# Kernel tuning notes

Hardware: AMD Instinct MI355X
Metric: run time of the kernel (lower is better)

The kernel has to match this reference:

```python
import jax, jax.numpy as jnp
import numpy as np

B, P, E, H = 2, 4096, 512, 8
D = E // H
EPS = 1e-5


def _layernorm2d(x, g, b):
    # LayerNorm over last two dims (patches, embed) jointly, per torch nn.LayerNorm([P, E])
    mu = jnp.mean(x, axis=(-2, -1), keepdims=True)
    var = jnp.mean(jnp.square(x - mu), axis=(-2, -1), keepdims=True)
    return (x - mu) * jax.lax.rsqrt(var + EPS) * g + b


def setup_inputs() -> dict:
    key = jax.random.key(0)
    ks = jax.random.split(key, 4)
    s_in = 1.0 / np.sqrt(E)
    s_hid = 1.0 / np.sqrt(3 * E)
    return {
        "x": jax.random.normal(ks[0], (B, P, E), dtype=jnp.float32),
        "g1": jnp.ones((P, E), jnp.float32),
        "b1": jnp.zeros((P, E), jnp.float32),
        "W1": jax.random.normal(ks[1], (3 * E, E), jnp.float32) * s_in,
        "g2": jnp.ones((P, E), jnp.float32),
        "b2": jnp.zeros((P, E), jnp.float32),
        "Wa": jax.random.normal(ks[2], (3 * E, E), jnp.float32) * s_in,
        "ba": jnp.zeros((3 * E,), jnp.float32),
        "Wb": jax.random.normal(ks[3], (E, 3 * E), jnp.float32) * s_hid,
        "bb": jnp.zeros((E,), jnp.float32),
    }


def reference(x, g1, b1, W1, g2, b2, Wa, ba, Wb, bb):
    # --- attention branch ---
    h = _layernorm2d(x, g1, b1)                      # [B,P,E]
    qkv = h @ W1.T                                   # [B,P,3E]
    qkv = qkv.reshape(B, P, 3, H, D).transpose(2, 0, 3, 1, 4)  # [3,B,H,P,D]
    q, k, v = qkv[0], qkv[1], qkv[2]
    scale = 1.0 / jnp.sqrt(jnp.float32(D))
    dp = jnp.einsum("bhqd,bhkd->bhqk", q, k) * scale  # [B,H,P,P]
    # NOTE: softmax over axis -2 (the query axis), as in the original code
    dp = jax.nn.softmax(dp, axis=-2)
    wv = jnp.einsum("bhqk,bhkd->bhqd", dp, v)        # [B,H,P,D]
    wv = wv.transpose(0, 2, 1, 3).reshape(B, P, E)   # [B,P,E]
    out1 = x + wv
    # --- MLP branch ---
    h2 = _layernorm2d(out1, g2, b2)
    h2 = jax.nn.gelu(h2 @ Wa.T + ba, approximate=False)
    h2 = jax.nn.gelu(h2 @ Wb.T + bb, approximate=False)
    return h2 + out1
```

## Files before the change

kernel.cpp:

```cpp
#include <hip/hip_runtime.h>
#include <math.h>

typedef __bf16 bf16x8 __attribute__((ext_vector_type(8)));
typedef __bf16 bf16x4 __attribute__((ext_vector_type(4)));
typedef short s16x4 __attribute__((ext_vector_type(4)));
typedef float f32x4 __attribute__((ext_vector_type(4)));
typedef unsigned int u32x2 __attribute__((ext_vector_type(2)));
typedef unsigned short u16;
typedef unsigned int u32;

__device__ __forceinline__ void gl_lds16(const void* g, void* l) {
  __builtin_amdgcn_global_load_lds(
      (const __attribute__((address_space(1))) void*)g,
      (__attribute__((address_space(3))) void*)l, 16, 0, 0);
}

__device__ __forceinline__ u16 f2bf(float x) {
  union { float f; u32 u; } v; v.f = x;
  u32 r = v.u + 0x7FFFu + ((v.u >> 16) & 1u);
  return (u16)(r >> 16);
}

__device__ __forceinline__ float bflo(u32 u) {
  union { float f; u32 v; } t; t.v = u << 16; return t.f;
}
__device__ __forceinline__ float bfhi(u32 u) {
  union { float f; u32 v; } t; t.v = u & 0xFFFF0000u; return t.f;
}

__device__ __forceinline__ u32 pack_bf2(float a, float b) {
  union { float f; u32 u; } ua, ub; ua.f = a; ub.f = b;
  return ((ua.u + 0x8000u) >> 16) | ((ub.u + 0x8000u) & 0xFFFF0000u);
}

__device__ __forceinline__ float expfast(float x) {
#if __has_builtin(__builtin_amdgcn_exp2f)
  return __builtin_amdgcn_exp2f(x);
#else
  return exp2f(x);
#endif
}

__device__ __forceinline__ f32x4 mfma16(bf16x4 a, bf16x4 b, f32x4 c) {
#if __has_builtin(__builtin_amdgcn_mfma_f32_16x16x16_bf16)
  return __builtin_amdgcn_mfma_f32_16x16x16_bf16(a, b, c, 0, 0, 0);
#else
  return __builtin_amdgcn_mfma_f32_16x16x16bf16_1k(
      __builtin_bit_cast(s16x4, a), __builtin_bit_cast(s16x4, b), c, 0, 0, 0);
#endif
}

__device__ __forceinline__ float gelu_f(float v) {
  return 0.5f * v * (1.0f + erff(v * 0.7071067811865475f));
}

__global__ void cast_lnred(const float* __restrict__ s0, const float* __restrict__ s1,
                           const float* __restrict__ s2, u16* __restrict__ d0,
                           u16* __restrict__ d1, u16* __restrict__ d2,
                           const float* __restrict__ x, float2* __restrict__ part) {
  int blk = blockIdx.x;
  if (blk < 2304) {
    const float* s; u16* d;
    if (blk < 768)       { s = s0; d = d0; }
    else if (blk < 1536) { s = s1; d = d1; blk -= 768; }
    else                 { s = s2; d = d2; blk -= 1536; }
    int i = blk * 256 + threadIdx.x;
    float4 v = ((const float4*)s)[i];
    uint2 o;
    o.x = (u32)f2bf(v.x) | ((u32)f2bf(v.y) << 16);
    o.y = (u32)f2bf(v.z) | ((u32)f2bf(v.w) << 16);
    ((uint2*)d)[i] = o;
    return;
  }
  blk -= 2304;
  int b = blk >> 7, ib = blk & 127;
  const float4* p = (const float4*)(x + (size_t)b * 2097152 + (size_t)ib * 16384);
  float s = 0.f, q = 0.f;
  #pragma unroll
  for (int i = 0; i < 16; i++) {
    float4 v = p[i * 256 + threadIdx.x];
    s += v.x + v.y + v.z + v.w;
    q += v.x * v.x + v.y * v.y + v.z * v.z + v.w * v.w;
  }
  #pragma unroll
  for (int off = 32; off; off >>= 1) { s += __shfl_down(s, off, 64); q += __shfl_down(q, off, 64); }
  __shared__ float ls[4], lq[4];
  int w = threadIdx.x >> 6;
  if ((threadIdx.x & 63) == 0) { ls[w] = s; lq[w] = q; }
  __syncthreads();
  if (threadIdx.x == 0)
    part[b * 128 + ib] =
        make_float2(ls[0] + ls[1] + ls[2] + ls[3], lq[0] + lq[1] + lq[2] + lq[3]);
}

__global__ void comb_lnred(const float* __restrict__ x, const u16* __restrict__ opart,
                           float* __restrict__ o1, float2* __restrict__ part) {
  int blk = blockIdx.x;
  size_t base = (size_t)blk * 4096;
  const uint2* oa = (const uint2*)opart;
  const uint2* ob = (const uint2*)(opart + 4194304);
  float s = 0.f, q = 0.f;
  #pragma unroll
  for (int i = 0; i < 16; i++) {
    size_t idx = base + i * 256 + threadIdx.x;
    float4 v = ((const float4*)x)[idx];
    uint2 a = oa[idx];
    uint2 c = ob[idx];
    v.x += bflo(a.x) + bflo(c.x);
    v.y += bfhi(a.x) + bfhi(c.x);
    v.z += bflo(a.y) + bflo(c.y);
    v.w += bfhi(a.y) + bfhi(c.y);
    ((float4*)o1)[idx] = v;
    s += v.x + v.y + v.z + v.w;
    q += v.x * v.x + v.y * v.y + v.z * v.z + v.w * v.w;
  }
  #pragma unroll
  for (int off = 32; off; off >>= 1) { s += __shfl_down(s, off, 64); q += __shfl_down(q, off, 64); }
  __shared__ float ls[4], lq[4];
  int w = threadIdx.x >> 6;
  if ((threadIdx.x & 63) == 0) { ls[w] = s; lq[w] = q; }
  __syncthreads();
  if (threadIdx.x == 0)
    part[blk] = make_float2(ls[0] + ls[1] + ls[2] + ls[3], lq[0] + lq[1] + lq[2] + lq[3]);
}

__global__ void ln_apply(const float* __restrict__ src, const float* __restrict__ g,
                         const float* __restrict__ bta, const float2* __restrict__ part,
                         u16* __restrict__ dst) {
  int i = blockIdx.x * 256 + threadIdx.x;
  int b = i >= 524288;
  int lane = threadIdx.x & 63;
  float2 a = part[b * 128 + lane], c2 = part[b * 128 + 64 + lane];
  float s = a.x + c2.x, q = a.y + c2.y;
  #pragma unroll
  for (int off = 32; off; off >>= 1) { s += __shfl_down(s, off, 64); q += __shfl_down(q, off, 64); }
  s = __shfl(s, 0, 64); q = __shfl(q, 0, 64);
  const float inv = 1.0f / 2097152.0f;
  float mu = s * inv;
  float rsig = rsqrtf(q * inv - mu * mu + 1e-5f);
  int r = i - b * 524288;
  float4 v = ((const float4*)src)[i];
  float4 gv = ((const float4*)g)[r];
  float4 bv = ((const float4*)bta)[r];
  float h0 = (v.x - mu) * rsig * gv.x + bv.x;
  float h1 = (v.y - mu) * rsig * gv.y + bv.y;
  float h2 = (v.z - mu) * rsig * gv.z + bv.z;
  float h3 = (v.w - mu) * rsig * gv.w + bv.w;
  uint2 o;
  o.x = (u32)f2bf(h0) | ((u32)f2bf(h1) << 16);
  o.y = (u32)f2bf(h2) | ((u32)f2bf(h3) << 16);
  ((uint2*)dst)[i] = o;
}

template <int MODE>
__global__ __launch_bounds__(256, 2)
void gemm_bt(const u16* __restrict__ A, const u16* __restrict__ Bm,
             const float* __restrict__ bias, const float* __restrict__ res,
             float* __restrict__ outf, u16* __restrict__ outb,
             int M, int N, int K) {
  __shared__ u16 As[128 * 32], Bs[128 * 32];
  const int tid = threadIdx.x;
  const int m0 = blockIdx.y * 128, n0 = blockIdx.x * 128;
  const int lane = tid & 63, w = tid >> 6;
  const int wm = (w >> 1) * 64, wn = (w & 1) * 64;
  const int c = lane & 15, quad = lane >> 4;
  const int arow = tid >> 2, acol = (tid & 3) * 8;

  const u16* gA = A + (size_t)(m0 + arow) * K + acol;
  const u16* gB = Bm + (size_t)(n0 + arow) * K + acol;
  u16* lA = As + tid * 8;
  u16* lB = Bs + tid * 8;

  f32x4 acc[4][4] = {};
  for (int kt = 0; kt < K; kt += 32) {
    gl_lds16(gA, lA);
    gl_lds16(gA + (size_t)64 * K, lA + 64 * 32);
    gl_lds16(gB, lB);
    gl_lds16(gB + (size_t)64 * K, lB + 64 * 32);
    gA += 32; gB += 32;
    __syncthreads();
    bf16x8 af[4], bf[4];
    #pragma unroll
    for (int i = 0; i < 4; i++) {
      af[i] = *(const bf16x8*)&As[(wm + i * 16 + c) * 32 + quad * 8];
      bf[i] = *(const bf16x8*)&Bs[(wn + i * 16 + c) * 32 + quad * 8];
    }
    #pragma unroll
    for (int i = 0; i < 4; i++)
      #pragma unroll
      for (int j = 0; j < 4; j++)
        acc[i][j] = __builtin_amdgcn_mfma_f32_16x16x32_bf16(af[i], bf[j], acc[i][j], 0, 0, 0);
    __syncthreads();
  }
  #pragma unroll
  for (int i = 0; i < 4; i++) {
    const int row0 = m0 + wm + i * 16 + quad * 4;
    #pragma unroll
    for (int j = 0; j < 4; j++) {
      const int col = n0 + wn + j * 16 + c;
      #pragma unroll
      for (int r = 0; r < 4; r++) {
        float v = acc[i][j][r];
        size_t oi = (size_t)(row0 + r) * N + col;
        if (MODE == 0 && col < 512) v *= 0.1803368801111204f;
        if (MODE == 1 || MODE == 2) v = gelu_f(v + bias[col]);
        if (MODE == 2) outf[oi] = v + res[oi];
        else           outb[oi] = f2bf(v);
      }
    }
  }
}

__global__ __launch_bounds__(256, 4)
void attn_pass1(const u16* __restrict__ qkv, float* __restrict__ rlpart) {
  __shared__ u16 Qs[2][2 * 128 * 32];
  const int tid = threadIdx.x;
  const int bh = blockIdx.y, b = bh >> 3, h = bh & 7;
  const int k0 = blockIdx.x * 128;
  const int lane = tid & 63, w = tid >> 6;
  const int wn = w * 32;
  const int c = lane & 15, quad = lane >> 4;
  const int arow = tid >> 2, acol = (tid & 3) * 8;

  bf16x8 bk[2][2];
  {
    const u16* Kg = qkv + ((size_t)(b * 4096 + k0 + wn + c)) * 1536 + 512 + h * 64 + quad * 8;
    #pragma unroll
    for (int j = 0; j < 2; j++)
      #pragma unroll
      for (int ks = 0; ks < 2; ks++)
        bk[j][ks] = *(const bf16x8*)(Kg + (size_t)j * 16 * 1536 + ks * 32);
  }
  const u16* Qg = qkv + ((size_t)(b * 4096 + blockIdx.z * 2048)) * 1536 + h * 64;

  #define STAGE_Q(t)                                                              \
    {                                                                             \
      u16* dst = Qs[(t) & 1];                                                     \
      const u16* src = Qg + (size_t)((t) * 128) * 1536;                           \
      _Pragma("unroll")                                                           \
      for (int ks = 0; ks < 2; ks++)                                              \
        _Pragma("unroll")                                                         \
        for (int rr = 0; rr < 128; rr += 64)                                      \
          gl_lds16(src + (size_t)(rr + arow) * 1536 + ks * 32 + acol,             \
                   dst + ks * 4096 + (rr + arow) * 32 + acol);                    \
    }

  STAGE_Q(0);
  float s0 = 0.f, s1 = 0.f;
  for (int t = 0; t < 16; t++) {
    __syncthreads();
    if (t + 1 < 16) STAGE_Q(t + 1);
    const u16* buf = Qs[t & 1];
    #pragma unroll
    for (int i = 0; i < 8; i++) {
      bf16x8 a0 = *(const bf16x8*)&buf[(i * 16 + c) * 32 + quad * 8];
      bf16x8 a1 = *(const bf16x8*)&buf[4096 + (i * 16 + c) * 32 + quad * 8];
      f32x4 acc0 = {}, acc1 = {};
      acc0 = __builtin_amdgcn_mfma_f32_16x16x32_bf16(a0, bk[0][0], acc0, 0, 0, 0);
      acc0 = __builtin_amdgcn_mfma_f32_16x16x32_bf16(a1, bk[0][1], acc0, 0, 0, 0);
      acc1 = __builtin_amdgcn_mfma_f32_16x16x32_bf16(a0, bk[1][0], acc1, 0, 0, 0);
      acc1 = __builtin_amdgcn_mfma_f32_16x16x32_bf16(a1, bk[1][1], acc1, 0, 0, 0);
      #pragma unroll
      for (int r = 0; r < 4; r++) {
        s0 += expfast(acc0[r]);
        s1 += expfast(acc1[r]);
      }
    }
  }
  #undef STAGE_Q
  s0 += __shfl_xor(s0, 16, 64); s0 += __shfl_xor(s0, 32, 64);
  s1 += __shfl_xor(s1, 16, 64); s1 += __shfl_xor(s1, 32, 64);
  if (quad == 0) {
    float* rp = rlpart + ((size_t)blockIdx.z * 16 + bh) * 4096 + k0 + wn;
    rp[c] = s0;
    rp[16 + c] = s1;
  }
}

__global__ void vtrans(const u16* __restrict__ qkv, const float* __restrict__ rlpart,
                       u16* __restrict__ vt) {
  __shared__ u16 t[64 * 66];
  __shared__ float rls[64];
  int bh = blockIdx.y, p0 = blockIdx.x * 64;
  int b = bh >> 3, h = bh & 7;
  const u16* src = qkv + ((size_t)(b * 4096 + p0)) * 1536 + 1024 + h * 64;
  int tid = threadIdx.x;
  if (tid < 64) {
    size_t idx = (size_t)bh * 4096 + p0 + tid;
    rls[tid] = 1.0f / (rlpart[idx] + rlpart[65536 + idx]);
  }
  __syncthreads();
  #pragma unroll
  for (int j = 0; j < 16; j++) {
    int idx = j * 256 + tid;
    int p = idx >> 6, d = idx & 63;
    union { float f; u32 u; } uv;
    uv.u = ((u32)src[(size_t)p * 1536 + d]) << 16;
    t[d * 66 + p] = f2bf(uv.f * rls[p]);
  }
  __syncthreads();
  u16* dst = vt + (size_t)bh * 262144 + (size_t)blockIdx.x * 4096;
  #pragma unroll
  for (int j = 0; j < 16; j++) {
    int idx = j * 256 + tid;
    int d = idx >> 6, p = idx & 63;
    dst[d * 64 + ((((p >> 3) & 7) ^ (d & 7)) << 3) + (p & 7)] = t[d * 66 + p];
  }
}

__global__ __launch_bounds__(256, 4)
void attn_pass2(const u16* __restrict__ qkv, const u16* __restrict__ vt,
                u16* __restrict__ opart) {
  __shared__ u16 Ks[2][2][2048];
  __shared__ u16 Vs[2][4096];
  const int tid = threadIdx.x;
  const int bh = blockIdx.y, b = bh >> 3, h = bh & 7;
  const int q0 = blockIdx.x * 128;
  const int kh = blockIdx.z;
  const int lane = tid & 63, w = tid >> 6;
  const int wq = w * 32;
  const int c = lane & 15, quad = lane >> 4;

  bf16x8 bq[2][2];
  {
    const u16* Qg = qkv + ((size_t)(b * 4096 + q0 + wq + c)) * 1536 + h * 64 + quad * 8;
    #pragma unroll
    for (int j = 0; j < 2; j++)
      #pragma unroll
      for (int ks = 0; ks < 2; ks++)
        bq[j][ks] = *(const bf16x8*)(Qg + (size_t)j * 16 * 1536 + ks * 32);
  }
  const u16* Kg = qkv + ((size_t)(b * 4096 + kh * 2048)) * 1536 + 512 + h * 64;
  const u16* Vg = vt + (size_t)bh * 262144 + (size_t)kh * 131072;

  #define STAGE_KV(t)                                                             \
    {                                                                             \
      const int buf_ = (t) & 1;                                                   \
      const int krow_ = (t) * 64 + (tid >> 2);                                    \
      _Pragma("unroll")                                                           \
      for (int ks = 0; ks < 2; ks++)                                              \
        gl_lds16(Kg + (size_t)krow_ * 1536 + ks * 32 + (tid & 3) * 8,             \
                 &Ks[buf_][ks][tid * 8]);                                         \
      gl_lds16(Vg + (t) * 4096 + tid * 8, &Vs[buf_][tid * 8]);                    \
      gl_lds16(Vg + (t) * 4096 + 2048 + tid * 8, &Vs[buf_][2048 + tid * 8]);      \
    }

  STAGE_KV(0);
  f32x4 oacc[2][4] = {};
  for (int t = 0; t < 32; t++) {
    __syncthreads();
    if (t + 1 < 32) STAGE_KV(t + 1);
    const int buf = t & 1;

    f32x4 sacc[4][2] = {};
    #pragma unroll
    for (int i = 0; i < 4; i++) {
      bf16x8 af0 = *(const bf16x8*)&Ks[buf][0][(i * 16 + c) * 32 + quad * 8];
      bf16x8 af1 = *(const bf16x8*)&Ks[buf][1][(i * 16 + c) * 32 + quad * 8];
      #pragma unroll
      for (int j = 0; j < 2; j++) {
        sacc[i][j] = __builtin_amdgcn_mfma_f32_16x16x32_bf16(af0, bq[j][0], sacc[i][j], 0, 0, 0);
        sacc[i][j] = __builtin_amdgcn_mfma_f32_16x16x32_bf16(af1, bq[j][1], sacc[i][j], 0, 0, 0);
      }
    }
    bf16x4 pa[4][2];
    #pragma unroll
    for (int i = 0; i < 4; i++)
      #pragma unroll
      for (int j = 0; j < 2; j++) {
        u32x2 pk;
        pk.x = pack_bf2(expfast(sacc[i][j][0]), expfast(sacc[i][j][1]));
        pk.y = pack_bf2(expfast(sacc[i][j][2]), expfast(sacc[i][j][3]));
        pa[i][j] = __builtin_bit_cast(bf16x4, pk);
      }
    #pragma unroll
    for (int kc = 0; kc < 4; kc++) {
      const int kb = 2 * kc + (quad >> 1);
      #pragma unroll
      for (int j2 = 0; j2 < 4; j2++) {
        const int d = j2 * 16 + c;
        bf16x4 vf = *(const bf16x4*)&Vs[buf][d * 64 + ((kb ^ (d & 7)) << 3) + 4 * (quad & 1)];
        oacc[0][j2] = mfma16(pa[kc][0], vf, oacc[0][j2]);
        oacc[1][j2] = mfma16(pa[kc][1], vf, oacc[1][j2]);
      }
    }
  }
  #undef STAGE_KV
  u16* op = opart + (size_t)kh * 4194304;
  #pragma unroll
  for (int i2 = 0; i2 < 2; i2++)
    #pragma unroll
    for (int j2 = 0; j2 < 4; j2++)
      #pragma unroll
      for (int r = 0; r < 4; r++) {
        const int q = q0 + wq + i2 * 16 + quad * 4 + r;
        const int d = j2 * 16 + c;
        op[((size_t)(b * 4096 + q)) * 512 + h * 64 + d] = f2bf(oacc[i2][j2][r]);
      }
}

extern "C" void kernel_launch(void* const* d_in, const int* in_sizes, int n_in,
                              void* d_out, int out_size, void* d_ws, size_t ws_size,
                              hipStream_t stream) {
  const float* x  = (const float*)d_in[0];
  const float* g1 = (const float*)d_in[1];
  const float* b1 = (const float*)d_in[2];
  const float* W1 = (const float*)d_in[3];
  const float* g2 = (const float*)d_in[4];
  const float* b2 = (const float*)d_in[5];
  const float* Wa = (const float*)d_in[6];
  const float* ba = (const float*)d_in[7];
  const float* Wb = (const float*)d_in[8];
  const float* bb = (const float*)d_in[9];
  float* out = (float*)d_out;

  char* ws = (char*)d_ws;
  u16* w1b   = (u16*)(ws);
  u16* wab   = (u16*)(ws + 1572864);
  u16* wbb   = (u16*)(ws + 3145728);
  u16* h1    = (u16*)(ws + 4718592);
  u16* qkv   = (u16*)(ws + 13107200);
  u16* vt    = (u16*)(ws + 38273024);
  u16* h2    = (u16*)(ws + 46661632);
  u16* mid   = (u16*)(ws + 55050240);
  float* o1  = (float*)(ws + 80478208);
  float2* part  = (float2*)(ws + 97255424);
  float* rlpart = (float*)(ws + 55050240);
  u16* opart    = (u16*)(ws + 55050240);

  cast_lnred<<<2560, 256, 0, stream>>>(W1, Wa, Wb, w1b, wab, wbb, x, part);
  ln_apply<<<4096, 256, 0, stream>>>(x, g1, b1, part, h1);

  gemm_bt<0><<<dim3(12, 64), 256, 0, stream>>>(h1, w1b, nullptr, nullptr, nullptr, qkv,
                                               8192, 1536, 512);
  attn_pass1<<<dim3(32, 16, 2), 256, 0, stream>>>(qkv, rlpart);
  vtrans<<<dim3(64, 16), 256, 0, stream>>>(qkv, rlpart, vt);
  attn_pass2<<<dim3(32, 16, 2), 256, 0, stream>>>(qkv, vt, opart);

  comb_lnred<<<256, 256, 0, stream>>>(x, opart, o1, part);
  ln_apply<<<4096, 256, 0, stream>>>(o1, g2, b2, part, h2);

  gemm_bt<1><<<dim3(12, 64), 256, 0, stream>>>(h2, wab, ba, nullptr, nullptr, mid,
                                               8192, 1536, 512);
  gemm_bt<2><<<dim3(4, 64), 256, 0, stream>>>(mid, wbb, bb, o1, out, nullptr,
                                              8192, 512, 1536);
}
```

Measured before the change: 363.8 us.

## Reformat V for direct register loads in attention and narrow final GEMM tile

The transposed V buffer is rewritten into a fragment-ordered layout, so attn_pass2 loads V operands straight from global memory into registers. This removes the LDS staging and its swizzle. A separate 128x64-tile GEMM kernel is added for the final MLP projection, doubling its block count from 256 to 512 to fill more compute units. The trade-off is that V reads now depend on cache and latency instead of being prefetched into LDS, and the narrower tile reuses data less.

```diff
diff --git a/kernel.cpp b/kernel.cpp
--- a/kernel.cpp
+++ b/kernel.cpp
@@ -155,8 +155,7 @@
 template <int MODE>
 __global__ __launch_bounds__(256, 2)
 void gemm_bt(const u16* __restrict__ A, const u16* __restrict__ Bm,
-             const float* __restrict__ bias, const float* __restrict__ res,
-             float* __restrict__ outf, u16* __restrict__ outb,
+             const float* __restrict__ bias, u16* __restrict__ outb,
              int M, int N, int K) {
   __shared__ u16 As[128 * 32], Bs[128 * 32];
   const int tid = threadIdx.x;
@@ -203,9 +202,63 @@
         float v = acc[i][j][r];
         size_t oi = (size_t)(row0 + r) * N + col;
         if (MODE == 0 && col < 512) v *= 0.1803368801111204f;
-        if (MODE == 1 || MODE == 2) v = gelu_f(v + bias[col]);
-        if (MODE == 2) outf[oi] = v + res[oi];
-        else           outb[oi] = f2bf(v);
+        if (MODE == 1) v = gelu_f(v + bias[col]);
+        outb[oi] = f2bf(v);
+      }
+    }
+  }
+}
+
+__global__ __launch_bounds__(256, 2)
+void gemm_bt2(const u16* __restrict__ A, const u16* __restrict__ Bm,
+              const float* __restrict__ bias, const float* __restrict__ res,
+              float* __restrict__ outf, int M, int N, int K) {
+  __shared__ u16 As[128 * 32], Bs[64 * 32];
+  const int tid = threadIdx.x;
+  const int m0 = blockIdx.y * 128, n0 = blockIdx.x * 64;
+  const int lane = tid & 63, w = tid >> 6;
+  const int wm = w * 32;
+  const int c = lane & 15, quad = lane >> 4;
+  const int arow = tid >> 2, acol = (tid & 3) * 8;
+
+  const u16* gA = A + (size_t)(m0 + arow) * K + acol;
+  const u16* gB = Bm + (size_t)(n0 + arow) * K + acol;
+  u16* lA = As + tid * 8;
+  u16* lB = Bs + tid * 8;
+
+  f32x4 acc[2][4] = {};
+  for (int kt = 0; kt < K; kt += 32) {
+    gl_lds16(gA, lA);
+    gl_lds16(gA + (size_t)64 * K, lA + 64 * 32);
+    if (arow < 64) gl_lds16(gB, lB);
+    gA += 32; gB += 32;
+    __syncthreads();
+    bf16x8 af[2], bf[4];
+    #pragma unroll
+    for (int i = 0; i < 2; i++)
+      af[i] = *(const bf16x8*)&As[(wm + i * 16 + c) * 32 + quad * 8];
+    #pragma unroll
+    for (int j = 0; j < 4; j++)
+      bf[j] = *(const bf16x8*)&Bs[(j * 16 + c) * 32 + quad * 8];
+    #pragma unroll
+    for (int i = 0; i < 2; i++)
+      #pragma unroll
+      for (int j = 0; j < 4; j++)
+        acc[i][j] = __builtin_amdgcn_mfma_f32_16x16x32_bf16(af[i], bf[j], acc[i][j], 0, 0, 0);
+    __syncthreads();
+  }
+  #pragma unroll
+  for (int i = 0; i < 2; i++) {
+    const int row0 = m0 + wm + i * 16 + quad * 4;
+    #pragma unroll
+    for (int j = 0; j < 4; j++) {
+      const int col = n0 + j * 16 + c;
+      #pragma unroll
+      for (int r = 0; r < 4; r++) {
+        float v = acc[i][j][r];
+        size_t oi = (size_t)(row0 + r) * N + col;
+        v = gelu_f(v + bias[col]);
+        outf[oi] = v + res[oi];
       }
     }
   }
@@ -279,7 +332,7 @@
 
 __global__ void vtrans(const u16* __restrict__ qkv, const float* __restrict__ rlpart,
                        u16* __restrict__ vt) {
-  __shared__ u16 t[64 * 66];
+  __shared__ u16 t[64 * 68];
   __shared__ float rls[64];
   int bh = blockIdx.y, p0 = blockIdx.x * 64;
   int b = bh >> 3, h = bh & 7;
@@ -296,15 +349,18 @@
     int p = idx >> 6, d = idx & 63;
     union { float f; u32 u; } uv;
     uv.u = ((u32)src[(size_t)p * 1536 + d]) << 16;
-    t[d * 66 + p] = f2bf(uv.f * rls[p]);
+    t[d * 68 + p] = f2bf(uv.f * rls[p]);
   }
   __syncthreads();
   u16* dst = vt + (size_t)bh * 262144 + (size_t)blockIdx.x * 4096;
   #pragma unroll
-  for (int j = 0; j < 16; j++) {
+  for (int j = 0; j < 4; j++) {
     int idx = j * 256 + tid;
-    int d = idx >> 6, p = idx & 63;
-    dst[d * 64 + ((((p >> 3) & 7) ^ (d & 7)) << 3) + (p & 7)] = t[d * 66 + p];
+    int d = idx & 63, kl = idx >> 6;
+    u32 a = *(const u32*)&t[d * 68 + 4 * kl];
+    u32 b2 = *(const u32*)&t[d * 68 + 4 * kl + 2];
+    uint2 o; o.x = a; o.y = b2;
+    *(uint2*)(dst + kl * 256 + d * 4) = o;
   }
 }
 
@@ -312,7 +368,6 @@
 void attn_pass2(const u16* __restrict__ qkv, const u16* __restrict__ vt,
                 u16* __restrict__ opart) {
   __shared__ u16 Ks[2][2][2048];
-  __shared__ u16 Vs[2][4096];
   const int tid = threadIdx.x;
   const int bh = blockIdx.y, b = bh >> 3, h = bh & 7;
   const int q0 = blockIdx.x * 128;
@@ -333,7 +388,7 @@
   const u16* Kg = qkv + ((size_t)(b * 4096 + kh * 2048)) * 1536 + 512 + h * 64;
   const u16* Vg = vt + (size_t)bh * 262144 + (size_t)kh * 131072;
 
-  #define STAGE_KV(t)                                                             \
+  #define STAGE_K(t)                                                              \
     {                                                                             \
       const int buf_ = (t) & 1;                                                   \
       const int krow_ = (t) * 64 + (tid >> 2);                                    \
@@ -341,15 +396,13 @@
       for (int ks = 0; ks < 2; ks++)                                              \
         gl_lds16(Kg + (size_t)krow_ * 1536 + ks * 32 + (tid & 3) * 8,             \
                  &Ks[buf_][ks][tid * 8]);                                         \
-      gl_lds16(Vg + (t) * 4096 + tid * 8, &Vs[buf_][tid * 8]);                    \
-      gl_lds16(Vg + (t) * 4096 + 2048 + tid * 8, &Vs[buf_][2048 + tid * 8]);      \
-    }
-
-  STAGE_KV(0);
+    }
+
+  STAGE_K(0);
   f32x4 oacc[2][4] = {};
   for (int t = 0; t < 32; t++) {
     __syncthreads();
-    if (t + 1 < 32) STAGE_KV(t + 1);
+    if (t + 1 < 32) STAGE_K(t + 1);
     const int buf = t & 1;
 
     f32x4 sacc[4][2] = {};
@@ -363,6 +416,13 @@
         sacc[i][j] = __builtin_amdgcn_mfma_f32_16x16x32_bf16(af1, bq[j][1], sacc[i][j], 0, 0, 0);
       }
     }
+    const u16* vbase = Vg + (size_t)t * 4096;
+    bf16x4 vf0[2][4];
+    #pragma unroll
+    for (int kc = 0; kc < 2; kc++)
+      #pragma unroll
+      for (int j2 = 0; j2 < 4; j2++)
+        vf0[kc][j2] = *(const bf16x4*)(vbase + (4 * kc + quad) * 256 + (j2 * 16 + c) * 4);
     bf16x4 pa[4][2];
     #pragma unroll
     for (int i = 0; i < 4; i++)
@@ -374,18 +434,27 @@
         pa[i][j] = __builtin_bit_cast(bf16x4, pk);
       }
     #pragma unroll
-    for (int kc = 0; kc < 4; kc++) {
-      const int kb = 2 * kc + (quad >> 1);
+    for (int kc = 0; kc < 2; kc++)
       #pragma unroll
       for (int j2 = 0; j2 < 4; j2++) {
-        const int d = j2 * 16 + c;
-        bf16x4 vf = *(const bf16x4*)&Vs[buf][d * 64 + ((kb ^ (d & 7)) << 3) + 4 * (quad & 1)];
-        oacc[0][j2] = mfma16(pa[kc][0], vf, oacc[0][j2]);
-        oacc[1][j2] = mfma16(pa[kc][1], vf, oacc[1][j2]);
-      }
-    }
-  }
-  #undef STAGE_KV
+        oacc[0][j2] = mfma16(pa[kc][0], vf0[kc][j2], oacc[0][j2]);
+        oacc[1][j2] = mfma16(pa[kc][1], vf0[kc][j2], oacc[1][j2]);
+      }
+    bf16x4 vf1[2][4];
+    #pragma unroll
+    for (int kc = 0; kc < 2; kc++)
+      #pragma unroll
+      for (int j2 = 0; j2 < 4; j2++)
+        vf1[kc][j2] = *(const bf16x4*)(vbase + (4 * (kc + 2) + quad) * 256 + (j2 * 16 + c) * 4);
+    #pragma unroll
+    for (int kc = 0; kc < 2; kc++)
+      #pragma unroll
+      for (int j2 = 0; j2 < 4; j2++) {
+        oacc[0][j2] = mfma16(pa[kc + 2][0], vf1[kc][j2], oacc[0][j2]);
+        oacc[1][j2] = mfma16(pa[kc + 2][1], vf1[kc][j2], oacc[1][j2]);
+      }
+  }
+  #undef STAGE_K
   u16* op = opart + (size_t)kh * 4194304;
   #pragma unroll
   for (int i2 = 0; i2 < 2; i2++)
@@ -431,8 +500,7 @@
   cast_lnred<<<2560, 256, 0, stream>>>(W1, Wa, Wb, w1b, wab, wbb, x, part);
   ln_apply<<<4096, 256, 0, stream>>>(x, g1, b1, part, h1);
 
-  gemm_bt<0><<<dim3(12, 64), 256, 0, stream>>>(h1, w1b, nullptr, nullptr, nullptr, qkv,
-                                               8192, 1536, 512);
+  gemm_bt<0><<<dim3(12, 64), 256, 0, stream>>>(h1, w1b, nullptr, qkv, 8192, 1536, 512);
   attn_pass1<<<dim3(32, 16, 2), 256, 0, stream>>>(qkv, rlpart);
   vtrans<<<dim3(64, 16), 256, 0, stream>>>(qkv, rlpart, vt);
   attn_pass2<<<dim3(32, 16, 2), 256, 0, stream>>>(qkv, vt, opart);
@@ -440,8 +508,6 @@
   comb_lnred<<<256, 256, 0, stream>>>(x, opart, o1, part);
   ln_apply<<<4096, 256, 0, stream>>>(o1, g2, b2, part, h2);
 
-  gemm_bt<1><<<dim3(12, 64), 256, 0, stream>>>(h2, wab, ba, nullptr, nullptr, mid,
-                                               8192, 1536, 512);
-  gemm_bt<2><<<dim3(4, 64), 256, 0, stream>>>(mid, wbb, bb, o1, out, nullptr,
-                                              8192, 512, 1536);
-}
+  gemm_bt<1><<<dim3(12, 64), 256, 0, stream>>>(h2, wab, ba, mid, 8192, 1536, 512);
+  gemm_bt2<<<dim3(8, 64), 256, 0, stream>>>(mid, wbb, bb, o1, out, 8192, 512, 1536);
+}
```

After: 365.2 us. Within noise of the previous version (+0.4%).
